# Kernel optimization log

Hardware: AMD Instinct MI355X
Metric: run time of the kernel (lower is better)

Reference implementation:

```python
import jax, jax.numpy as jnp
import numpy as np

N_NODES = 50000
N_EDGES = 1000000
N_LAYERS = 3

# Equivariant tensor-product coupling constants (component-normalized CG, Cartesian form):
#  - 1o x 1o -> 0e :  (v . Y1)/sqrt(3) = v . n            (Y1 = sqrt(3) n)
#  - 0e x 1o -> 1o :  s * Y1 = sqrt(3) s n
#  - 1o x 2e -> 1o :  sqrt(9/2) * ((v.n) n - v/3)          (Y2 ~ sqrt(15/2)(n n^T - I/3))
C121 = 2.1213203435596424  # sqrt(4.5)
SQRT3 = 1.7320508075688772


def _forward(positions, node_features, Wss, Wsv, Wus, Wuv, W1, W2, W3, Wds, Wdv,
             senders, receivers):
    n_nodes = positions.shape[0]
    vec = positions[receivers] - positions[senders]                 # [E,3]
    length = jnp.linalg.norm(vec, axis=-1)                          # [E]
    safe = jnp.where(length == 0.0, 1.0, length)
    nhat = vec / safe[:, None]                                      # unit edge vectors

    # radial embedding: bessel(n=8, x_max=1) * poly_envelope(5,2)
    kk = jnp.arange(1, 9, dtype=positions.dtype)                    # [8]
    bess = jnp.sqrt(2.0) * jnp.sin(jnp.pi * kk[None, :] * length[:, None]) / safe[:, None]
    x = length
    poly = 1.0 - 28.0 * x**6 + 48.0 * x**7 - 21.0 * x**8
    env = jnp.where(x < 1.0, poly, 0.0)
    radial = jnp.where(length[:, None] == 0.0, 0.0, bess * env[:, None])   # [E,8]

    s = node_features[:, :1]                                        # [N,1]   0e
    v = node_features[:, 1:].reshape(-1, 2, 3)                      # [N,2,3] 2x1o

    for l in range(N_LAYERS):
        # self connection: (0e + 2x1o) -> (3x0e + 2x1o)
        s_sc = s @ Wss[l]                                           # [N,3]
        v_sc = jnp.einsum('nmc,mk->nkc', v, Wsv[l]) / jnp.sqrt(2.0) # [N,2,3]
        # linear_up (irreps-preserving)
        su = s @ Wus[l]
        vu = jnp.einsum('nmc,mk->nkc', v, Wuv[l]) / jnp.sqrt(2.0)
        # gather onto edges
        se = su[senders]                                            # [E,1]
        ve = vu[senders]                                            # [E,2,3]
        # tensor product with spherical harmonics (filtered to 0e,1o)
        vdotn = jnp.einsum('emc,ec->em', ve, nhat)                  # [E,2]
        tp0 = vdotn                                                 # 1o x 1o -> 0e
        pc = C121 * (vdotn[:, :, None] * nhat[:, None, :] - ve / 3.0)  # 1o x 2e -> 1o, [E,2,3]
        pb = SQRT3 * se[:, :, None] * nhat[:, None, :]              # 0e x 1o -> 1o, [E,1,3]
        msg_s = jnp.concatenate([se, tp0], axis=1)                  # [E,3]  3x0e
        msg_v = jnp.concatenate([ve, pc, pb], axis=1)               # [E,5,3] 5x1o
        # radial MLP -> one mixing scalar per irrep (8 = 3 + 5)
        h = jax.nn.swish(radial @ W1[l] / jnp.sqrt(8.0))
        h = jax.nn.swish(h @ W2[l] / jnp.sqrt(64.0))
        mix = h @ W3[l] / jnp.sqrt(64.0)                            # [E,8]
        msg_s = msg_s * mix[:, :3]
        msg_v = msg_v * mix[:, 3:, None]
        # scatter-add into nodes (avg_num_neighbors = 1.0 -> no rescale)
        agg_s = jax.ops.segment_sum(msg_s, receivers, num_segments=n_nodes)
        agg_v = jax.ops.segment_sum(msg_v.reshape(-1, 15), receivers,
                                    num_segments=n_nodes).reshape(-1, 5, 3)
        # linear_down: (3x0e + 5x1o) -> (3x0e + 2x1o)
        sd = agg_s @ Wds[l] / jnp.sqrt(3.0)
        vd = jnp.einsum('nmc,mk->nkc', agg_v, Wdv[l]) / jnp.sqrt(5.0)
        st = sd + s_sc                                              # [N,3]
        vt = vd + v_sc                                              # [N,2,3]
        # gate: 1 even scalar (swish), 2 even gates (swish) gating the 2x1o
        s = jax.nn.swish(st[:, :1])
        v = vt * jax.nn.swish(st[:, 1:3])[:, :, None]
    # displacement = first 1o vector of the output features
    return v[:, 0, :]                                               # [N,3]


def setup_inputs() -> dict:
    key = jax.random.key(0)
    ks = jax.random.split(key, 13)
    inp = {
        'positions': jax.random.normal(ks[0], (N_NODES, 3), jnp.float32) * 0.15,
        'node_features': jax.random.normal(ks[1], (N_NODES, 7), jnp.float32),
        'senders': jax.random.randint(ks[2], (N_EDGES,), 0, N_NODES, jnp.int32),
        'receivers': jax.random.randint(ks[3], (N_EDGES,), 0, N_NODES, jnp.int32),
        'Wss': jax.random.normal(ks[4], (N_LAYERS, 1, 3), jnp.float32),
        'Wsv': jax.random.normal(ks[5], (N_LAYERS, 2, 2), jnp.float32),
        'Wus': jax.random.normal(ks[6], (N_LAYERS, 1, 1), jnp.float32),
        'Wuv': jax.random.normal(ks[7], (N_LAYERS, 2, 2), jnp.float32),
        'W1': jax.random.normal(ks[8], (N_LAYERS, 8, 64), jnp.float32),
        'W2': jax.random.normal(ks[9], (N_LAYERS, 64, 64), jnp.float32),
        'W3': jax.random.normal(ks[10], (N_LAYERS, 64, 8), jnp.float32),
        'Wds': jax.random.normal(ks[11], (N_LAYERS, 3, 3), jnp.float32),
        'Wdv': jax.random.normal(ks[12], (N_LAYERS, 5, 2), jnp.float32),
    }
    return inp


def reference(positions, node_features, senders, receivers,
              Wss, Wsv, Wus, Wuv, W1, W2, W3, Wds, Wdv):
    return _forward(positions, node_features, Wss, Wsv, Wus, Wuv,
                    W1, W2, W3, Wds, Wdv, senders, receivers)
```

## Files before the change

kernel.cpp:

```cpp
#include <hip/hip_runtime.h>
#include <hip/hip_bf16.h>
#include <math.h>

#define NN 50000
#define NE 1000000

typedef __attribute__((ext_vector_type(8))) short bf16x8;
typedef __attribute__((ext_vector_type(4))) float f32x4;

constexpr float kC121    = 2.1213203435596424f;
constexpr float kSqrt3   = 1.7320508075688772f;
constexpr float kInvSqrt2= 0.7071067811865475f;
constexpr float kInvSqrt8= 0.35355339059327373f;
constexpr float kInvSqrt3= 0.5773502691896258f;
constexpr float kInvSqrt5= 0.4472135954999579f;
constexpr float kSqrt2   = 1.4142135623730951f;
constexpr float kPi      = 3.14159265358979323846f;

__device__ __forceinline__ float swishf(float x){
    return x * __builtin_amdgcn_rcpf(1.0f + __expf(-x));
}
__device__ __forceinline__ unsigned short f2bf(float f){
    unsigned int u = __float_as_uint(f);
    u += 0x7fffu + ((u>>16)&1u);
    return (unsigned short)(u>>16);
}
__device__ __forceinline__ unsigned int pk2(float a, float b){
    union { __hip_bfloat162 h; unsigned int u; } cv;
    cv.h = __float22bfloat162_rn(make_float2(a,b));
    return cv.u;
}

#define REP64A(M) M(0) M(1) M(2) M(3) M(4) M(5) M(6) M(7) M(8) M(9) \
 M(10) M(11) M(12) M(13) M(14) M(15) M(16) M(17) M(18) M(19) \
 M(20) M(21) M(22) M(23) M(24) M(25) M(26) M(27) M(28) M(29) \
 M(30) M(31) M(32) M(33) M(34) M(35) M(36) M(37) M(38) M(39) \
 M(40) M(41) M(42) M(43) M(44) M(45) M(46) M(47) M(48) M(49) \
 M(50) M(51) M(52) M(53) M(54) M(55) M(56) M(57) M(58) M(59) \
 M(60) M(61) M(62) M(63)
#define REP64B(M) M(0) M(1) M(2) M(3) M(4) M(5) M(6) M(7) M(8) M(9) \
 M(10) M(11) M(12) M(13) M(14) M(15) M(16) M(17) M(18) M(19) \
 M(20) M(21) M(22) M(23) M(24) M(25) M(26) M(27) M(28) M(29) \
 M(30) M(31) M(32) M(33) M(34) M(35) M(36) M(37) M(38) M(39) \
 M(40) M(41) M(42) M(43) M(44) M(45) M(46) M(47) M(48) M(49) \
 M(50) M(51) M(52) M(53) M(54) M(55) M(56) M(57) M(58) M(59) \
 M(60) M(61) M(62) M(63)
#define STAGE1(J) float h_##J; { const float* w = W1T + (J)*8; \
    float a = fmaf(r0,w[0],fmaf(r1,w[1],fmaf(r2,w[2],fmaf(r3,w[3], \
              fmaf(r4,w[4],fmaf(r5,w[5],fmaf(r6,w[6],r7*w[7]))))))); \
    h_##J = swishf(a*kInvSqrt8); }
#define DECLACC(J) float acc_##J = 0.f;
#define UPD(J) acc_##J = fmaf(hk, w2r[J], acc_##J);
#define KSTEP(K) { float hk = h_##K; const float* w2r = W2 + (K)*64; REP64B(UPD) }
#define S3(J) { float a = swishf(acc_##J*0.125f); const float* w3 = W3 + (J)*8; \
    m0=fmaf(a,w3[0],m0); m1=fmaf(a,w3[1],m1); m2=fmaf(a,w3[2],m2); m3=fmaf(a,w3[3],m3); \
    m4=fmaf(a,w3[4],m4); m5=fmaf(a,w3[5],m5); m6=fmaf(a,w3[6],m6); m7=fmaf(a,w3[7],m7); }
#define MLP_BODY \
    float m0=0.f,m1=0.f,m2=0.f,m3=0.f,m4=0.f,m5=0.f,m6=0.f,m7=0.f; \
    { REP64A(STAGE1) REP64A(DECLACC) REP64A(KSTEP) REP64A(S3) } \
    m0*=0.125f; m1*=0.125f; m2*=0.125f; m3*=0.125f; \
    m4*=0.125f; m5*=0.125f; m6*=0.125f; m7*=0.125f;


__global__ void transpose_w1(const float* __restrict__ W1, float* __restrict__ W1T){
    int i = blockIdx.x*blockDim.x + threadIdx.x;
    if (i < 3*8*64){
        int l = i/512, r = i%512; int k = r/64, j = r%64;
        W1T[l*512 + j*8 + k] = W1[i];
    }
}

__global__ void build_frags(const float* __restrict__ W1, const float* __restrict__ W2,
                            const float* __restrict__ W3,
                            unsigned short* __restrict__ W1F,
                            unsigned short* __restrict__ W2F,
                            unsigned short* __restrict__ W3F){
    int t = blockIdx.x*blockDim.x + threadIdx.x;
    if (t < 3*4*64*8){
        int i=t&7, lane=(t>>3)&63, jt=(t>>9)&3, l=t>>11;
        int g=lane>>4, c=lane&15;
        int k=8*g+i, j=16*jt+c;
        float v = (k<8) ? W1[l*512 + k*64 + j]*kInvSqrt8 : 0.f;
        W1F[t] = f2bf(v);
    }
    if (t < 3*2*4*64*8){
        int i=t&7, lane=(t>>3)&63, jt=(t>>9)&3, kt=(t>>11)&1, l=t>>12;
        int g=lane>>4, c=lane&15;
        int k=32*kt+8*g+i, j=16*jt+c;
        W2F[t] = f2bf(W2[l*4096 + k*64 + j]*0.125f);
    }
    if (t < 3*2*64*8){
        int i=t&7, lane=(t>>3)&63, kt=(t>>9)&1, l=t>>10;
        int g=lane>>4, c=lane&15;
        int k=32*kt+8*g+i;
        float v = (c<8) ? W3[l*512 + k*8 + c]*0.125f : 0.f;
        W3F[t] = f2bf(v);
    }
}

__global__ void hist_rcv(const int* __restrict__ rcv, int* __restrict__ cnt){
    int e = blockIdx.x*blockDim.x + threadIdx.x;
    if (e < NE) atomicAdd(&cnt[rcv[e]], 1);
}

__global__ void exscan(const int* __restrict__ cnt, int* __restrict__ rowptr,
                       int* __restrict__ wcur){
    __shared__ int wsum[16];
    __shared__ int carry_s;
    int tid = threadIdx.x;
    int lane = tid & 63, wv = tid >> 6;
    if (tid==0) carry_s = 0;
    __syncthreads();
    for (int base=0; base<NN; base+=4096){
        int i0 = base + tid*4;
        int v0 = (i0+0<NN)?cnt[i0+0]:0;
        int v1 = (i0+1<NN)?cnt[i0+1]:0;
        int v2 = (i0+2<NN)?cnt[i0+2]:0;
        int v3 = (i0+3<NN)?cnt[i0+3]:0;
        int t = v0+v1+v2+v3;
        int sc = t;
        #pragma unroll
        for (int off=1; off<64; off<<=1){
            int u = __shfl_up(sc, off, 64);
            if (lane >= off) sc += u;
        }
        if (lane==63) wsum[wv] = sc;
        __syncthreads();
        if (wv==0 && lane<16){
            int ws = wsum[lane];
            #pragma unroll
            for (int off=1; off<16; off<<=1){
                int u = __shfl_up(ws, off, 64);
                if (lane>=off) ws += u;
            }
            wsum[lane] = ws;
        }
        __syncthreads();
        int carry = carry_s;
        int wbase = (wv==0)?0:wsum[wv-1];
        int ex = carry + wbase + (sc - t);
        if (i0+0<NN){ rowptr[i0+0]=ex; wcur[i0+0]=ex; } ex += v0;
        if (i0+1<NN){ rowptr[i0+1]=ex; wcur[i0+1]=ex; } ex += v1;
        if (i0+2<NN){ rowptr[i0+2]=ex; wcur[i0+2]=ex; } ex += v2;
        if (i0+3<NN){ rowptr[i0+3]=ex; wcur[i0+3]=ex; }
        __syncthreads();
        if (tid==0) carry_s = carry + wsum[15];
        __syncthreads();
    }
    if (threadIdx.x==0) rowptr[NN] = carry_s;
}

__global__ void scatter_edges(const int* __restrict__ snd, const int* __restrict__ rcv,
                              int* __restrict__ wcur,
                              int* __restrict__ slot, int* __restrict__ snd_s){
    int e = blockIdx.x*blockDim.x + threadIdx.x;
    if (e >= NE) return;
    int pos = atomicAdd(&wcur[rcv[e]], 1);
    slot[e] = pos;
    snd_s[pos] = snd[e];
}

__global__ void edge_geom(const float* __restrict__ pos,
                          const int* __restrict__ snd,
                          const int* __restrict__ rcv,
                          const int* __restrict__ slot,
                          float* __restrict__ nhat,
                          float* __restrict__ radial_f,
                          unsigned short* __restrict__ radial_bf){
    int e = blockIdx.x*blockDim.x + threadIdx.x;
    if (e >= NE) return;
    int s = snd[e], r = rcv[e];
    float vx = pos[r*3+0]-pos[s*3+0];
    float vy = pos[r*3+1]-pos[s*3+1];
    float vz = pos[r*3+2]-pos[s*3+2];
    float len = sqrtf(vx*vx+vy*vy+vz*vz);
    float safe = (len==0.f)?1.f:len;
    float inv = 1.f/safe;
    int p = slot ? slot[e] : e;
    nhat[p*3+0]=vx*inv; nhat[p*3+1]=vy*inv; nhat[p*3+2]=vz*inv;
    float x = len;
    float x3=x*x*x, x6=x3*x3, x7=x6*x, x8=x7*x;
    float poly = 1.f - 28.f*x6 + 48.f*x7 - 21.f*x8;
    float env = (x<1.f)?poly:0.f;
    float c = kSqrt2*env*inv;
    float s1, c1;
    __sincosf(kPi*len, &s1, &c1);
    float tc = 2.f*c1;
    float sk_m1 = 0.f, sk = s1;
    float zero = (len==0.f)?0.f:1.f;
    float rv[8];
    #pragma unroll
    for (int k=1;k<=8;k++){
        rv[k-1] = sk*c*zero;
        float nxt = tc*sk - sk_m1;
        sk_m1 = sk; sk = nxt;
    }
    if (radial_bf){
        uint4 pk;
        pk.x = pk2(rv[0],rv[1]); pk.y = pk2(rv[2],rv[3]);
        pk.z = pk2(rv[4],rv[5]); pk.w = pk2(rv[6],rv[7]);
        *(uint4*)(radial_bf + (size_t)p*8) = pk;
    } else {
        #pragma unroll
        for (int k=0;k<8;k++) radial_f[p*8+k] = rv[k];
    }
}

__global__ void node_init_pre(const float* __restrict__ nf,
                              const float* __restrict__ Wss, const float* __restrict__ Wsv,
                              const float* __restrict__ Wus, const float* __restrict__ Wuv,
                              float* __restrict__ s_sc, float* __restrict__ v_sc,
                              float* __restrict__ su, float* __restrict__ vu){
    int n = blockIdx.x*blockDim.x + threadIdx.x;
    if (n >= NN) return;
    float sv = nf[n*7];
    float vv[6];
    #pragma unroll
    for (int i=0;i<6;i++) vv[i] = nf[n*7+1+i];
    #pragma unroll
    for (int i=0;i<3;i++) s_sc[n*3+i] = sv*Wss[i];
    #pragma unroll
    for (int k=0;k<2;k++)
        #pragma unroll
        for (int c=0;c<3;c++)
            v_sc[n*6+k*3+c] = (vv[c]*Wsv[0*2+k] + vv[3+c]*Wsv[1*2+k]) * kInvSqrt2;
    su[n] = sv * Wus[0];
    #pragma unroll
    for (int k=0;k<2;k++)
        #pragma unroll
        for (int c=0;c<3;c++)
            vu[n*6+k*3+c] = (vv[c]*Wuv[0*2+k] + vv[3+c]*Wuv[1*2+k]) * kInvSqrt2;
}

__global__ void __launch_bounds__(256) edge_msg_mfma(
    const int* __restrict__ snd_s,
    const float* __restrict__ nhat, const unsigned short* __restrict__ radial_bf,
    const float* __restrict__ su, const float* __restrict__ vu,
    const unsigned short* __restrict__ W1F, const unsigned short* __restrict__ W2F,
    const unsigned short* __restrict__ W3F,
    float* __restrict__ msg){
    __shared__ unsigned short hbuf_s[4][16*72];
    __shared__ float mixbuf_s[4][64*12];
    int tid = threadIdx.x;
    int w = tid>>6, l = tid&63;
    int g = l>>4, c = l&15;
    long base = ((long)blockIdx.x*4 + w)*64;
    if (base >= NE) return;
    char* hrow = (char*)hbuf_s[w] + c*144;
    float* mixbuf = mixbuf_s[w];
    int swz = (c&7)<<4;

    bf16x8 w1f[4], w2f[2][4], w3f[2];
    #pragma unroll
    for (int jt=0;jt<4;jt++)
        w1f[jt] = *(const bf16x8*)(W1F + (jt*64 + l)*8);
    #pragma unroll
    for (int kt=0;kt<2;kt++)
        #pragma unroll
        for (int jt=0;jt<4;jt++)
            w2f[kt][jt] = *(const bf16x8*)(W2F + ((kt*4+jt)*64 + l)*8);
    #pragma unroll
    for (int kt=0;kt<2;kt++)
        w3f[kt] = *(const bf16x8*)(W3F + (kt*64 + l)*8);

    #pragma unroll 1
    for (int nt=0; nt<4; ++nt){
        bf16x8 brad = {0,0,0,0,0,0,0,0};
        if (g==0)
            brad = *(const bf16x8*)(radial_bf + (size_t)(base + 16*nt + c)*8);
        #pragma unroll
        for (int jt=0;jt<4;jt++){
            f32x4 z = {0.f,0.f,0.f,0.f};
            f32x4 d1 = __builtin_amdgcn_mfma_f32_16x16x32_bf16(w1f[jt], brad, z, 0,0,0);
            uint2 pk;
            pk.x = pk2(swishf(d1[0]), swishf(d1[1]));
            pk.y = pk2(swishf(d1[2]), swishf(d1[3]));
            *(uint2*)(hrow + ((32*jt + 8*g) ^ swz)) = pk;
        }
        bf16x8 bh0 = *(const bf16x8*)(hrow + ((16*g) ^ swz));
        bf16x8 bh1 = *(const bf16x8*)(hrow + ((64 + 16*g) ^ swz));
        #pragma unroll
        for (int jt=0;jt<4;jt++){
            f32x4 z = {0.f,0.f,0.f,0.f};
            f32x4 d2 = __builtin_amdgcn_mfma_f32_16x16x32_bf16(w2f[0][jt], bh0, z, 0,0,0);
            d2 = __builtin_amdgcn_mfma_f32_16x16x32_bf16(w2f[1][jt], bh1, d2, 0,0,0);
            uint2 pk;
            pk.x = pk2(swishf(d2[0]), swishf(d2[1]));
            pk.y = pk2(swishf(d2[2]), swishf(d2[3]));
            *(uint2*)(hrow + ((32*jt + 8*g) ^ swz)) = pk;
        }
        bf16x8 ch0 = *(const bf16x8*)(hrow + ((16*g) ^ swz));
        bf16x8 ch1 = *(const bf16x8*)(hrow + ((64 + 16*g) ^ swz));
        f32x4 z3 = {0.f,0.f,0.f,0.f};
        f32x4 mx = __builtin_amdgcn_mfma_f32_16x16x32_bf16(w3f[0], ch0, z3, 0,0,0);
        mx = __builtin_amdgcn_mfma_f32_16x16x32_bf16(w3f[1], ch1, mx, 0,0,0);
        if (g < 2)
            *(f32x4*)(mixbuf + (16*nt + c)*12 + 4*g) = mx;
    }

    long e = base + l;
    const float* mr = mixbuf + l*12;
    float mm0=mr[0], mm1=mr[1], mm2=mr[2], mm3=mr[3];
    float mm4=mr[4], mm5=mr[5], mm6=mr[6], mm7=mr[7];
    int sn = snd_s[e];
    float se = su[sn];
    float ve[6];
    #pragma unroll
    for (int i=0;i<6;i++) ve[i] = vu[sn*6+i];
    float nh[3];
    #pragma unroll
    for (int i=0;i<3;i++) nh[i] = nhat[e*3+i];
    float vd0 = ve[0]*nh[0]+ve[1]*nh[1]+ve[2]*nh[2];
    float vd1 = ve[3]*nh[0]+ve[4]*nh[1]+ve[5]*nh[2];
    float* mp = msg + e*18;
    mp[0] = se *mm0;
    mp[1] = vd0*mm1;
    mp[2] = vd1*mm2;
    #pragma unroll
    for (int i=0;i<3;i++){
        mp[3 +i] = ve[i]*mm3;
        mp[6 +i] = ve[3+i]*mm4;
        mp[9 +i] = kC121*(vd0*nh[i]-ve[i]*(1.f/3.f))*mm5;
        mp[12+i] = kC121*(vd1*nh[i]-ve[3+i]*(1.f/3.f))*mm6;
        mp[15+i] = kSqrt3*se*nh[i]*mm7;
    }
}

__global__ void agg_update(const float* __restrict__ msg, const int* __restrict__ rowptr,
                           const float* __restrict__ Wds, const float* __restrict__ Wdv,
                           float* __restrict__ s_sc, float* __restrict__ v_sc,
                           float* __restrict__ su, float* __restrict__ vu,
                           const float* __restrict__ Wss_n, const float* __restrict__ Wsv_n,
                           const float* __restrict__ Wus_n, const float* __restrict__ Wuv_n,
                           float* __restrict__ out, int is_last){
    int n = blockIdx.x*blockDim.x + threadIdx.x;
    if (n >= NN) return;
    float acc[18];
    #pragma unroll
    for (int c=0;c<18;c++) acc[c]=0.f;
    int b = rowptr[n], e2 = rowptr[n+1];
    for (int sIdx=b; sIdx<e2; ++sIdx){
        const float* mp = msg + (size_t)sIdx*18;
        #pragma unroll
        for (int c=0;c<18;c++) acc[c] += mp[c];
    }
    float st[3];
    #pragma unroll
    for (int i=0;i<3;i++)
        st[i] = (acc[0]*Wds[0*3+i]+acc[1]*Wds[1*3+i]+acc[2]*Wds[2*3+i])*kInvSqrt3 + s_sc[n*3+i];
    float vt[6];
    #pragma unroll
    for (int k=0;k<2;k++)
        #pragma unroll
        for (int c=0;c<3;c++){
            float a = 0.f;
            #pragma unroll
            for (int m=0;m<5;m++) a += acc[3+m*3+c]*Wdv[m*2+k];
            vt[k*3+c] = a*kInvSqrt5 + v_sc[n*6+k*3+c];
        }
    float snew = swishf(st[0]);
    float g1 = swishf(st[1]), g2 = swishf(st[2]);
    float nv[6];
    #pragma unroll
    for (int c=0;c<3;c++){ nv[c] = vt[c]*g1; nv[3+c] = vt[3+c]*g2; }
    if (is_last){
        #pragma unroll
        for (int c=0;c<3;c++) out[n*3+c] = nv[c];
    } else {
        #pragma unroll
        for (int i=0;i<3;i++) s_sc[n*3+i] = snew*Wss_n[i];
        #pragma unroll
        for (int k=0;k<2;k++)
            #pragma unroll
            for (int c=0;c<3;c++)
                v_sc[n*6+k*3+c] = (nv[c]*Wsv_n[0*2+k] + nv[3+c]*Wsv_n[1*2+k]) * kInvSqrt2;
        su[n] = snew * Wus_n[0];
        #pragma unroll
        for (int k=0;k<2;k++)
            #pragma unroll
            for (int c=0;c<3;c++)
                vu[n*6+k*3+c] = (nv[c]*Wuv_n[0*2+k] + nv[3+c]*Wuv_n[1*2+k]) * kInvSqrt2;
    }
}

__global__ void node_init(const float* __restrict__ nf,
                          float* __restrict__ s, float* __restrict__ v){
    int n = blockIdx.x*blockDim.x + threadIdx.x;
    if (n >= NN) return;
    s[n] = nf[n*7];
    #pragma unroll
    for (int i=0;i<6;i++) v[n*6+i] = nf[n*7+1+i];
}

__global__ void node_pre(const float* __restrict__ s, const float* __restrict__ v,
                         const float* __restrict__ Wss, const float* __restrict__ Wsv,
                         const float* __restrict__ Wus, const float* __restrict__ Wuv,
                         float* __restrict__ s_sc, float* __restrict__ v_sc,
                         float* __restrict__ su, float* __restrict__ vu){
    int n = blockIdx.x*blockDim.x + threadIdx.x;
    if (n >= NN) return;
    float sv = s[n];
    float vv[6];
    #pragma unroll
    for (int i=0;i<6;i++) vv[i] = v[n*6+i];
    #pragma unroll
    for (int i=0;i<3;i++) s_sc[n*3+i] = sv*Wss[i];
    #pragma unroll
    for (int k=0;k<2;k++)
        #pragma unroll
        for (int c=0;c<3;c++)
            v_sc[n*6+k*3+c] = (vv[c]*Wsv[0*2+k] + vv[3+c]*Wsv[1*2+k]) * kInvSqrt2;
    su[n] = sv * Wus[0];
    #pragma unroll
    for (int k=0;k<2;k++)
        #pragma unroll
        for (int c=0;c<3;c++)
            vu[n*6+k*3+c] = (vv[c]*Wuv[0*2+k] + vv[3+c]*Wuv[1*2+k]) * kInvSqrt2;
}

__global__ void __launch_bounds__(256, 3) edge_msg_atomic(
    const int* __restrict__ snd, const int* __restrict__ rcv,
    const float* __restrict__ nhat, const float* __restrict__ radial,
    const float* __restrict__ su, const float* __restrict__ vu,
    const float* __restrict__ W1T, const float* __restrict__ W2,
    const float* __restrict__ W3,
    float* __restrict__ aggs, float* __restrict__ aggv){
    int e = blockIdx.x*blockDim.x + threadIdx.x;
    if (e >= NE) return;

    float r0 = radial[e*8+0], r1 = radial[e*8+1], r2 = radial[e*8+2], r3 = radial[e*8+3];
    float r4 = radial[e*8+4], r5 = radial[e*8+5], r6 = radial[e*8+6], r7 = radial[e*8+7];

    MLP_BODY

    int sn = snd[e], rn = rcv[e];
    float se = su[sn];
    float ve[6];
    #pragma unroll
    for (int i=0;i<6;i++) ve[i] = vu[sn*6+i];
    float nh[3];
    #pragma unroll
    for (int c=0;c<3;c++) nh[c] = nhat[e*3+c];
    float vd0 = ve[0]*nh[0]+ve[1]*nh[1]+ve[2]*nh[2];
    float vd1 = ve[3]*nh[0]+ve[4]*nh[1]+ve[5]*nh[2];

    atomicAdd(&aggs[rn*3+0], se *m0);
    atomicAdd(&aggs[rn*3+1], vd0*m1);
    atomicAdd(&aggs[rn*3+2], vd1*m2);
    #pragma unroll
    for (int c=0;c<3;c++){
        atomicAdd(&aggv[rn*15+0 +c], ve[c]*m3);
        atomicAdd(&aggv[rn*15+3 +c], ve[3+c]*m4);
        atomicAdd(&aggv[rn*15+6 +c], kC121*(vd0*nh[c]-ve[c]*(1.f/3.f))*m5);
        atomicAdd(&aggv[rn*15+9 +c], kC121*(vd1*nh[c]-ve[3+c]*(1.f/3.f))*m6);
        atomicAdd(&aggv[rn*15+12+c], kSqrt3*se*nh[c]*m7);
    }
}

__global__ void node_post_split(const float* __restrict__ aggs, const float* __restrict__ aggv,
                                const float* __restrict__ Wds, const float* __restrict__ Wdv,
                                const float* __restrict__ s_sc, const float* __restrict__ v_sc,
                                float* __restrict__ s, float* __restrict__ v,
                                float* __restrict__ out, int is_last){
    int n = blockIdx.x*blockDim.x + threadIdx.x;
    if (n >= NN) return;
    float as[3];
    #pragma unroll
    for (int j=0;j<3;j++) as[j] = aggs[n*3+j];
    float st[3];
    #pragma unroll
    for (int i=0;i<3;i++)
        st[i] = (as[0]*Wds[0*3+i]+as[1]*Wds[1*3+i]+as[2]*Wds[2*3+i])*kInvSqrt3 + s_sc[n*3+i];
    float vt[6];
    #pragma unroll
    for (int k=0;k<2;k++)
        #pragma unroll
        for (int c=0;c<3;c++){
            float acc = 0.f;
            #pragma unroll
            for (int m=0;m<5;m++) acc += aggv[n*15+m*3+c]*Wdv[m*2+k];
            vt[k*3+c] = acc*kInvSqrt5 + v_sc[n*6+k*3+c];
        }
    float snew = swishf(st[0]);
    float g1 = swishf(st[1]), g2 = swishf(st[2]);
    s[n] = snew;
    #pragma unroll
    for (int c=0;c<3;c++){
        float v0 = vt[c]*g1;
        float v1 = vt[3+c]*g2;
        v[n*6+c]   = v0;
        v[n*6+3+c] = v1;
        if (is_last) out[n*3+c] = v0;
    }
}

extern "C" void kernel_launch(void* const* d_in, const int* in_sizes, int n_in,
                              void* d_out, int out_size, void* d_ws, size_t ws_size,
                              hipStream_t stream){
    const float* pos = (const float*)d_in[0];
    const float* nf  = (const float*)d_in[1];
    const int*   snd = (const int*)d_in[2];
    const int*   rcv = (const int*)d_in[3];
    const float* Wss = (const float*)d_in[4];
    const float* Wsv = (const float*)d_in[5];
    const float* Wus = (const float*)d_in[6];
    const float* Wuv = (const float*)d_in[7];
    const float* W1  = (const float*)d_in[8];
    const float* W2  = (const float*)d_in[9];
    const float* W3  = (const float*)d_in[10];
    const float* Wds = (const float*)d_in[11];
    const float* Wdv = (const float*)d_in[12];
    float* out = (float*)d_out;

    dim3 blk(256);
    dim3 gE((NE+255)/256), gN((NN+255)/256);

    size_t need_sorted = ((size_t)NE*21 + (size_t)NN*16)*4
                       + ((size_t)NE*8 + 21504)*2
                       + ((size_t)NN*3 + 1 + (size_t)NE*2)*4 + 64;

    if (ws_size >= need_sorted){
        float* p = (float*)d_ws;
        float* nhat_s  = p; p += (size_t)NE*3;
        float* msg     = p; p += (size_t)NE*18;
        float* s_sc    = p; p += NN*3;
        float* v_sc    = p; p += NN*6;
        float* su      = p; p += NN;
        float* vu      = p; p += NN*6;
        unsigned short* wp = (unsigned short*)p;
        unsigned short* radial_bf = wp;    wp += (size_t)NE*8;
        unsigned short* W1F = wp;          wp += 3*4*64*8;
        unsigned short* W2F = wp;          wp += 3*2*4*64*8;
        unsigned short* W3F = wp;          wp += 3*2*64*8;
        int* ip = (int*)wp;
        int* cnt    = ip; ip += NN;
        int* rowptr = ip; ip += NN+1;
        int* wcur   = ip; ip += NN;
        int* slot   = ip; ip += NE;
        int* snd_s  = ip; ip += NE;

        build_frags<<<dim3(48), blk, 0, stream>>>(W1, W2, W3, W1F, W2F, W3F);
        hipMemsetAsync(cnt, 0, NN*sizeof(int), stream);
        hist_rcv<<<gE, blk, 0, stream>>>(rcv, cnt);
        exscan<<<dim3(1), dim3(1024), 0, stream>>>(cnt, rowptr, wcur);
        scatter_edges<<<gE, blk, 0, stream>>>(snd, rcv, wcur, slot, snd_s);
        edge_geom<<<gE, blk, 0, stream>>>(pos, snd, rcv, slot, nhat_s, nullptr, radial_bf);
        node_init_pre<<<gN, blk, 0, stream>>>(nf, Wss, Wsv, Wus, Wuv, s_sc, v_sc, su, vu);
        dim3 gW((NE/64 + 3)/4);
        for (int l=0;l<3;l++){
            edge_msg_mfma<<<gW, blk, 0, stream>>>(
                snd_s, nhat_s, radial_bf, su, vu,
                W1F + l*2048, W2F + l*4096, W3F + l*1024, msg);
            int nl = (l<2) ? l+1 : 0;
            agg_update<<<gN, blk, 0, stream>>>(
                msg, rowptr, Wds+l*9, Wdv+l*10,
                s_sc, v_sc, su, vu,
                Wss+nl*3, Wsv+nl*4, Wus+nl, Wuv+nl*4,
                out, (l==2)?1:0);
        }
    } else {
        float* p = (float*)d_ws;
        float* nhat   = p; p += (size_t)NE*3;
        float* radial = p; p += (size_t)NE*8;
        float* s      = p; p += NN;
        float* v      = p; p += NN*6;
        float* s_sc   = p; p += NN*3;
        float* v_sc   = p; p += NN*6;
        float* su     = p; p += NN;
        float* vu     = p; p += NN*6;
        float* aggs   = p; p += NN*3;
        float* aggv   = p; p += NN*15;
        float* W1T    = p; p += 1536;

        transpose_w1<<<dim3((1536+255)/256), blk, 0, stream>>>(W1, W1T);
        edge_geom<<<gE, blk, 0, stream>>>(pos, snd, rcv, nullptr, nhat, radial, nullptr);
        node_init<<<gN, blk, 0, stream>>>(nf, s, v);
        for (int l=0;l<3;l++){
            node_pre<<<gN, blk, 0, stream>>>(
                s, v, Wss+l*3, Wsv+l*4, Wus+l, Wuv+l*4, s_sc, v_sc, su, vu);
            hipMemsetAsync(aggs, 0, NN*3*sizeof(float), stream);
            hipMemsetAsync(aggv, 0, NN*15*sizeof(float), stream);
            edge_msg_atomic<<<gE, blk, 0, stream>>>(
                snd, rcv, nhat, radial, su, vu,
                W1T+l*512, W2+l*4096, W3+l*512, aggs, aggv);
            node_post_split<<<gN, blk, 0, stream>>>(
                aggs, aggv, Wds+l*9, Wdv+l*10, s_sc, v_sc, s, v, out, (l==2)?1:0);
        }
    }
}
```

Measured before the change: 479.5 us.

## Pack per-edge data into 32-byte records and fuse edge scatter into geometry

```diff
diff --git a/kernel.cpp b/kernel.cpp
--- a/kernel.cpp
+++ b/kernel.cpp
@@ -30,6 +30,12 @@
     cv.h = __float22bfloat162_rn(make_float2(a,b));
     return cv.u;
 }
+
+struct __align__(16) EdgeRec {
+    uint4 rad;
+    float nx, ny, nz;
+    int   sn;
+};
 
 #define REP64A(M) M(0) M(1) M(2) M(3) M(4) M(5) M(6) M(7) M(8) M(9) \
  M(10) M(11) M(12) M(13) M(14) M(15) M(16) M(17) M(18) M(19) \
@@ -98,13 +104,13 @@
     }
 }
 
-__global__ void hist_rcv(const int* __restrict__ rcv, int* __restrict__ cnt){
+__global__ void hist_rank(const int* __restrict__ rcv, int* __restrict__ cnt,
+                          int* __restrict__ lrank){
     int e = blockIdx.x*blockDim.x + threadIdx.x;
-    if (e < NE) atomicAdd(&cnt[rcv[e]], 1);
-}
-
-__global__ void exscan(const int* __restrict__ cnt, int* __restrict__ rowptr,
-                       int* __restrict__ wcur){
+    if (e < NE) lrank[e] = atomicAdd(&cnt[rcv[e]], 1);
+}
+
+__global__ void exscan(const int* __restrict__ cnt, int* __restrict__ rowptr){
     __shared__ int wsum[16];
     __shared__ int carry_s;
     int tid = threadIdx.x;
@@ -139,10 +145,10 @@
         int carry = carry_s;
         int wbase = (wv==0)?0:wsum[wv-1];
         int ex = carry + wbase + (sc - t);
-        if (i0+0<NN){ rowptr[i0+0]=ex; wcur[i0+0]=ex; } ex += v0;
-        if (i0+1<NN){ rowptr[i0+1]=ex; wcur[i0+1]=ex; } ex += v1;
-        if (i0+2<NN){ rowptr[i0+2]=ex; wcur[i0+2]=ex; } ex += v2;
-        if (i0+3<NN){ rowptr[i0+3]=ex; wcur[i0+3]=ex; }
+        if (i0+0<NN) rowptr[i0+0]=ex; ex += v0;
+        if (i0+1<NN) rowptr[i0+1]=ex; ex += v1;
+        if (i0+2<NN) rowptr[i0+2]=ex; ex += v2;
+        if (i0+3<NN) rowptr[i0+3]=ex;
         __syncthreads();
         if (tid==0) carry_s = carry + wsum[15];
         __syncthreads();
@@ -150,23 +156,12 @@
     if (threadIdx.x==0) rowptr[NN] = carry_s;
 }
 
-__global__ void scatter_edges(const int* __restrict__ snd, const int* __restrict__ rcv,
-                              int* __restrict__ wcur,
-                              int* __restrict__ slot, int* __restrict__ snd_s){
-    int e = blockIdx.x*blockDim.x + threadIdx.x;
-    if (e >= NE) return;
-    int pos = atomicAdd(&wcur[rcv[e]], 1);
-    slot[e] = pos;
-    snd_s[pos] = snd[e];
-}
-
-__global__ void edge_geom(const float* __restrict__ pos,
-                          const int* __restrict__ snd,
-                          const int* __restrict__ rcv,
-                          const int* __restrict__ slot,
-                          float* __restrict__ nhat,
-                          float* __restrict__ radial_f,
-                          unsigned short* __restrict__ radial_bf){
+__global__ void edge_geom_rec(const float* __restrict__ pos,
+                              const int* __restrict__ snd,
+                              const int* __restrict__ rcv,
+                              const int* __restrict__ rowptr,
+                              const int* __restrict__ lrank,
+                              EdgeRec* __restrict__ rec){
     int e = blockIdx.x*blockDim.x + threadIdx.x;
     if (e >= NE) return;
     int s = snd[e], r = rcv[e];
@@ -176,8 +171,6 @@
     float len = sqrtf(vx*vx+vy*vy+vz*vz);
     float safe = (len==0.f)?1.f:len;
     float inv = 1.f/safe;
-    int p = slot ? slot[e] : e;
-    nhat[p*3+0]=vx*inv; nhat[p*3+1]=vy*inv; nhat[p*3+2]=vz*inv;
     float x = len;
     float x3=x*x*x, x6=x3*x3, x7=x6*x, x8=x7*x;
     float poly = 1.f - 28.f*x6 + 48.f*x7 - 21.f*x8;
@@ -195,15 +188,13 @@
         float nxt = tc*sk - sk_m1;
         sk_m1 = sk; sk = nxt;
     }
-    if (radial_bf){
-        uint4 pk;
-        pk.x = pk2(rv[0],rv[1]); pk.y = pk2(rv[2],rv[3]);
-        pk.z = pk2(rv[4],rv[5]); pk.w = pk2(rv[6],rv[7]);
-        *(uint4*)(radial_bf + (size_t)p*8) = pk;
-    } else {
-        #pragma unroll
-        for (int k=0;k<8;k++) radial_f[p*8+k] = rv[k];
-    }
+    EdgeRec rc;
+    rc.rad.x = pk2(rv[0],rv[1]); rc.rad.y = pk2(rv[2],rv[3]);
+    rc.rad.z = pk2(rv[4],rv[5]); rc.rad.w = pk2(rv[6],rv[7]);
+    rc.nx = vx*inv; rc.ny = vy*inv; rc.nz = vz*inv;
+    rc.sn = s;
+    int p = rowptr[r] + lrank[e];
+    rec[p] = rc;
 }
 
 __global__ void node_init_pre(const float* __restrict__ nf,
@@ -233,8 +224,7 @@
 }
 
 __global__ void __launch_bounds__(256) edge_msg_mfma(
-    const int* __restrict__ snd_s,
-    const float* __restrict__ nhat, const unsigned short* __restrict__ radial_bf,
+    const EdgeRec* __restrict__ rec,
     const float* __restrict__ su, const float* __restrict__ vu,
     const unsigned short* __restrict__ W1F, const unsigned short* __restrict__ W2F,
     const unsigned short* __restrict__ W3F,
@@ -267,7 +257,7 @@
     for (int nt=0; nt<4; ++nt){
         bf16x8 brad = {0,0,0,0,0,0,0,0};
         if (g==0)
-            brad = *(const bf16x8*)(radial_bf + (size_t)(base + 16*nt + c)*8);
+            brad = *(const bf16x8*)&rec[base + 16*nt + c].rad;
         #pragma unroll
         for (int jt=0;jt<4;jt++){
             f32x4 z = {0.f,0.f,0.f,0.f};
@@ -299,17 +289,15 @@
     }
 
     long e = base + l;
+    EdgeRec r = rec[e];
     const float* mr = mixbuf + l*12;
     float mm0=mr[0], mm1=mr[1], mm2=mr[2], mm3=mr[3];
     float mm4=mr[4], mm5=mr[5], mm6=mr[6], mm7=mr[7];
-    int sn = snd_s[e];
-    float se = su[sn];
+    float se = su[r.sn];
     float ve[6];
     #pragma unroll
-    for (int i=0;i<6;i++) ve[i] = vu[sn*6+i];
-    float nh[3];
-    #pragma unroll
-    for (int i=0;i<3;i++) nh[i] = nhat[e*3+i];
+    for (int i=0;i<6;i++) ve[i] = vu[r.sn*6+i];
+    float nh[3] = { r.nx, r.ny, r.nz };
     float vd0 = ve[0]*nh[0]+ve[1]*nh[1]+ve[2]*nh[2];
     float vd1 = ve[3]*nh[0]+ve[4]*nh[1]+ve[5]*nh[2];
     float* mp = msg + e*18;
@@ -380,6 +368,39 @@
             #pragma unroll
             for (int c=0;c<3;c++)
                 vu[n*6+k*3+c] = (nv[c]*Wuv_n[0*2+k] + nv[3+c]*Wuv_n[1*2+k]) * kInvSqrt2;
+    }
+}
+
+__global__ void edge_geom_flat(const float* __restrict__ pos,
+                               const int* __restrict__ snd,
+                               const int* __restrict__ rcv,
+                               float* __restrict__ nhat,
+                               float* __restrict__ radial){
+    int e = blockIdx.x*blockDim.x + threadIdx.x;
+    if (e >= NE) return;
+    int s = snd[e], r = rcv[e];
+    float vx = pos[r*3+0]-pos[s*3+0];
+    float vy = pos[r*3+1]-pos[s*3+1];
+    float vz = pos[r*3+2]-pos[s*3+2];
+    float len = sqrtf(vx*vx+vy*vy+vz*vz);
+    float safe = (len==0.f)?1.f:len;
+    float inv = 1.f/safe;
+    nhat[e*3+0]=vx*inv; nhat[e*3+1]=vy*inv; nhat[e*3+2]=vz*inv;
+    float x = len;
+    float x3=x*x*x, x6=x3*x3, x7=x6*x, x8=x7*x;
+    float poly = 1.f - 28.f*x6 + 48.f*x7 - 21.f*x8;
+    float env = (x<1.f)?poly:0.f;
+    float c = kSqrt2*env*inv;
+    float s1, c1;
+    __sincosf(kPi*len, &s1, &c1);
+    float tc = 2.f*c1;
+    float sk_m1 = 0.f, sk = s1;
+    float zero = (len==0.f)?0.f:1.f;
+    #pragma unroll
+    for (int k=1;k<=8;k++){
+        radial[e*8+k-1] = sk*c*zero;
+        float nxt = tc*sk - sk_m1;
+        sk_m1 = sk; sk = nxt;
     }
 }
 
@@ -515,41 +536,38 @@
     dim3 blk(256);
     dim3 gE((NE+255)/256), gN((NN+255)/256);
 
-    size_t need_sorted = ((size_t)NE*21 + (size_t)NN*16)*4
-                       + ((size_t)NE*8 + 21504)*2
-                       + ((size_t)NN*3 + 1 + (size_t)NE*2)*4 + 64;
+    size_t need_sorted = ((size_t)NE*18 + (size_t)NN*16)*4
+                       + (size_t)NE*32
+                       + 21504*2
+                       + ((size_t)NN*2 + 1 + (size_t)NE)*4 + 64;
 
     if (ws_size >= need_sorted){
         float* p = (float*)d_ws;
-        float* nhat_s  = p; p += (size_t)NE*3;
         float* msg     = p; p += (size_t)NE*18;
         float* s_sc    = p; p += NN*3;
         float* v_sc    = p; p += NN*6;
         float* su      = p; p += NN;
         float* vu      = p; p += NN*6;
-        unsigned short* wp = (unsigned short*)p;
-        unsigned short* radial_bf = wp;    wp += (size_t)NE*8;
+        EdgeRec* rec   = (EdgeRec*)p;
+        unsigned short* wp = (unsigned short*)(rec + NE);
         unsigned short* W1F = wp;          wp += 3*4*64*8;
         unsigned short* W2F = wp;          wp += 3*2*4*64*8;
         unsigned short* W3F = wp;          wp += 3*2*64*8;
         int* ip = (int*)wp;
         int* cnt    = ip; ip += NN;
         int* rowptr = ip; ip += NN+1;
-        int* wcur   = ip; ip += NN;
-        int* slot   = ip; ip += NE;
-        int* snd_s  = ip; ip += NE;
+        int* lrank  = ip; ip += NE;
 
         build_frags<<<dim3(48), blk, 0, stream>>>(W1, W2, W3, W1F, W2F, W3F);
         hipMemsetAsync(cnt, 0, NN*sizeof(int), stream);
-        hist_rcv<<<gE, blk, 0, stream>>>(rcv, cnt);
-        exscan<<<dim3(1), dim3(1024), 0, stream>>>(cnt, rowptr, wcur);
-        scatter_edges<<<gE, blk, 0, stream>>>(snd, rcv, wcur, slot, snd_s);
-        edge_geom<<<gE, blk, 0, stream>>>(pos, snd, rcv, slot, nhat_s, nullptr, radial_bf);
+        hist_rank<<<gE, blk, 0, stream>>>(rcv, cnt, lrank);
+        exscan<<<dim3(1), dim3(1024), 0, stream>>>(cnt, rowptr);
+        edge_geom_rec<<<gE, blk, 0, stream>>>(pos, snd, rcv, rowptr, lrank, rec);
         node_init_pre<<<gN, blk, 0, stream>>>(nf, Wss, Wsv, Wus, Wuv, s_sc, v_sc, su, vu);
         dim3 gW((NE/64 + 3)/4);
         for (int l=0;l<3;l++){
             edge_msg_mfma<<<gW, blk, 0, stream>>>(
-                snd_s, nhat_s, radial_bf, su, vu,
+                rec, su, vu,
                 W1F + l*2048, W2F + l*4096, W3F + l*1024, msg);
             int nl = (l<2) ? l+1 : 0;
             agg_update<<<gN, blk, 0, stream>>>(
@@ -573,7 +591,7 @@
         float* W1T    = p; p += 1536;
 
         transpose_w1<<<dim3((1536+255)/256), blk, 0, stream>>>(W1, W1T);
-        edge_geom<<<gE, blk, 0, stream>>>(pos, snd, rcv, nullptr, nhat, radial, nullptr);
+        edge_geom_flat<<<gE, blk, 0, stream>>>(pos, snd, rcv, nhat, radial);
         node_init<<<gN, blk, 0, stream>>>(nf, s, v);
         for (int l=0;l<3;l++){
             node_pre<<<gN, blk, 0, stream>>>(
```

Result: faster. 385.8 us (-19.5%).
